# Performance work log

Measured on AMD Instinct MI355X. Metric: run time of the kernel, lower is better.

The kernel has to match this reference:

```python
import jax, jax.numpy as jnp
import numpy as np

L, M, DCUT, HL = 8, 8, 6, 2   # lattice rows, cols, bond dim, local Hilbert dim
N = L * M                     # nqubits
B = 32768                     # batch of spin configurations


def setup_inputs() -> dict:
    key = jax.random.key(0)
    ks = jax.random.split(key, 8)
    s = 0.1
    return {
        "parm_M_h": jax.random.normal(ks[0], (L, M, HL, DCUT, DCUT), jnp.float32) * s,
        "parm_M_v": jax.random.normal(ks[1], (L, M, HL, DCUT, DCUT), jnp.float32) * s,
        "parm_v":   jax.random.normal(ks[2], (L, M, HL, DCUT), jnp.float32) * s,
        "parm_T":   jax.random.normal(ks[3], (L, M, HL, DCUT, DCUT, DCUT), jnp.float32) * s,
        "parm_w":   jax.random.normal(ks[4], (L, M, DCUT), jnp.float32) * s,
        "parm_c":   jnp.zeros((L, M), jnp.float32),
        "parm_eta": jax.random.normal(ks[5], (L, M, DCUT), jnp.float32),
        "x":        jax.random.randint(ks[6], (B, N), 0, 2, jnp.int32),  # occupation bits 0/1
    }


def _snake_ij():
    # snake traversal: row i left->right if i even, right->left if i odd
    i = np.repeat(np.arange(L), M)
    jm = np.tile(np.arange(M), L)
    j = np.where(i % 2 == 0, jm, M - 1 - jm)
    return i, j


def _forward(parm_M_h, parm_M_v, parm_v, parm_T, parm_w, parm_c, parm_eta, x):
    target = x.T.astype(jnp.int32)               # (N, B) bits, qubit k visited at scan step k
    ii, jj = _snake_ij()
    # gather per-site params in snake scan order -> leading axis N
    Mh = parm_M_h[ii, jj]; Mv = parm_M_v[ii, jj]; V = parm_v[ii, jj]
    T = parm_T[ii, jj];    W = parm_w[ii, jj];    C = parm_c[ii, jj]
    Eta = parm_eta[ii, jj]
    jcol = jnp.asarray(jj, jnp.int32)            # column index per step (vertical state slot)
    row_start = jnp.asarray(np.arange(N) % M == 0)

    def step(carry, xs):
        h_h, v_state, amp, phi = carry
        Mh_k, Mv_k, V_k, T_k, W_k, C_k, eta_k, t_k, j_k, rs = xs
        # left boundary (ones) at the start of each row
        h_h = jnp.where(rs, 1.0, h_h)                                  # (dcut, B)
        h_v = jax.lax.dynamic_index_in_dim(v_state, j_k, 0, keepdims=False)  # (dcut, B)
        # update_h: residual small einsums ('abc,bd->acd' in torch)
        hh2 = h_h[None] + jnp.einsum('aoc,cb->aob', Mh_k, h_h)          # (hl, dcut, B)
        hv2 = h_v[None] + jnp.einsum('aoc,cb->aob', Mv_k, h_v)
        tt = jnp.einsum('aocd,cb,db->aob', T_k, h_h, h_v)               # tensor term
        h_full = hh2 + hv2 + tt + V_k[:, :, None]
        # normalize hidden per sample for numerical stability
        h_full = h_full / jnp.sqrt(jnp.sum(h_full * h_full, axis=(0, 1), keepdims=True) + 1e-12)
        # conditional probabilities P(s) ~ sum_o eta_o^2 h[s,o]^2
        q = jnp.einsum('o,aob->ab', eta_k * eta_k, h_full * h_full)     # (hl, B)
        prob = q / jnp.sum(q, axis=0, keepdims=True)
        sel = (t_k == 1)
        p_sel = jnp.where(sel, prob[1], prob[0])
        h_sel = jnp.where(sel[None, :], h_full[1], h_full[0])           # (dcut, B)
        amp = amp * jnp.sqrt(p_sel)
        phi = phi + jnp.einsum('o,ob->b', W_k, h_sel) + C_k             # regular phase accumulation
        v_state = jax.lax.dynamic_update_index_in_dim(v_state, h_sel, j_k, 0)
        return (h_sel, v_state, amp, phi), None

    h0 = jnp.ones((DCUT, B), jnp.float32)
    v0 = jnp.zeros((M, DCUT, B), jnp.float32)   # bottom boundary: zeros
    amp0 = jnp.ones((B,), jnp.float32)
    phi0 = jnp.zeros((B,), jnp.float32)
    (_, _, amp, phi), _ = jax.lax.scan(
        step, (h0, v0, amp0, phi0),
        (Mh, Mv, V, T, W, C, Eta, target, jcol, row_start))
    return amp, phi


def reference(parm_M_h, parm_M_v, parm_v, parm_T, parm_w, parm_c, parm_eta, x):
    amp, phi = _forward(parm_M_h, parm_M_v, parm_v, parm_T, parm_w, parm_c, parm_eta, x)
    # psi = amp * exp(i*phi)
    return amp * jnp.cos(phi) + 1j * (amp * jnp.sin(phi))
```

## Files before the change

### kernel.cpp

```cpp
#include <hip/hip_runtime.h>
#include <hip/hip_fp16.h>
#include <math.h>


#define NQ  64
#define BT  256
#define SPB 64
#define CHUNK_U 5184

typedef _Float16 h2v __attribute__((ext_vector_type(2)));
typedef __fp16  p2v __attribute__((ext_vector_type(2)));
union H2U { unsigned u; h2v h; __half2 hh; };

static __device__ __forceinline__ h2v pack2(float a, float b) {
    p2v p = __builtin_amdgcn_cvt_pkrtz(a, b);
    h2v r; __builtin_memcpy(&r, &p, sizeof(r));
    return r;
}
static __device__ __forceinline__ h2v u2h(unsigned u) {
    h2v r; __builtin_memcpy(&r, &u, sizeof(r));
    return r;
}
static __device__ __forceinline__ unsigned h2u(h2v h) {
    unsigned r; __builtin_memcpy(&r, &h, sizeof(r));
    return r;
}

#define DPPF(x, ctrl) __int_as_float(__builtin_amdgcn_update_dpp(            \
    __float_as_int(x), __float_as_int(x), (ctrl), 0xF, 0xF, false))
#define QP_XOR1 0xB1
#define QP_XOR2 0x4E
#define QP_BC0  0x00
#define QP_BC1  0x55

#if defined(__has_builtin)
#  if __has_builtin(__builtin_amdgcn_rcpf)
#    define FAST_RCP(x) __builtin_amdgcn_rcpf(x)
#  else
#    define FAST_RCP(x) (1.0f / (x))
#  endif
#  if __has_builtin(__builtin_amdgcn_rsqf)
#    define FAST_RSQ(x) __builtin_amdgcn_rsqf(x)
#  else
#    define FAST_RSQ(x) rsqrtf(x)
#  endif
#  if __has_builtin(__builtin_amdgcn_fdot2)
#    define HAS_FDOT2 1
#  endif
#else
#  define FAST_RCP(x) (1.0f / (x))
#  define FAST_RSQ(x) rsqrtf(x)
#endif

static __device__ __forceinline__ float fdot2u(unsigned a, h2v b, float c) {
#ifdef HAS_FDOT2
    H2U u; u.u = a;
    return __builtin_amdgcn_fdot2(u.h, b, c, false);
#else
    H2U u; u.u = a;
    return fmaf((float)u.h.x, (float)b.x, fmaf((float)u.h.y, (float)b.y, c));
#endif
}

__global__ void repack_k(
    const float* __restrict__ Mh, const float* __restrict__ Mv,
    const float* __restrict__ Vp, const float* __restrict__ Tp,
    const float* __restrict__ Wp, const float* __restrict__ Cp,
    const float* __restrict__ Ep, unsigned* __restrict__ ws)
{
    const int ch = blockIdx.x;
    const int t  = threadIdx.x;
    unsigned* Tm = ws + ch * CHUNK_U;
    float*    VE = reinterpret_cast<float*>(Tm + 4608);
    uint4*    Wl = reinterpret_cast<uint4*>(Tm + 4608 + 512);

    const float2* gT = reinterpret_cast<const float2*>(Tp + ch * 6912);
    for (int p = t; p < 3456; p += BT) {
        int site = p / 216, rr = p - site * 216;
        int row = rr / 18,  w  = rr - row * 18;
        float2 v = gT[p];
        H2U hu; hu.hh = __floats2half2_rn(v.x, v.y);
        Tm[(site * 12 + row) * 24 + w] = hu.u;
    }
    const float2* gH = reinterpret_cast<const float2*>(Mh + ch * 1152);
    const float2* gV = reinterpret_cast<const float2*>(Mv + ch * 1152);
    for (int p = t; p < 576; p += BT) {
        int site = p / 36, rr = p - site * 36;
        int row = rr / 3,  w  = rr - row * 3;
        int o_r = row - ((row >= 6) ? 6 : 0);
        float2 vh = gH[p], vv2 = gV[p];
        if ((o_r >> 1) == w) {
            if (o_r & 1) { vh.y += 1.f; vv2.y += 1.f; }
            else         { vh.x += 1.f; vv2.x += 1.f; }
        }
        H2U a; a.hh = __floats2half2_rn(vh.x, vh.y);
        H2U c; c.hh = __floats2half2_rn(vv2.x, vv2.y);
        Tm[(site * 12 + row) * 24 + 18 + w] = a.u;
        Tm[(site * 12 + row) * 24 + 21 + w] = c.u;
    }
    if (t < 192) {
        int site = t / 12, q = t - site * 12;
        int sb = q / 3,    c = q - sb * 3;
        VE[(site * 4 + sb) * 8 + c] = Vp[ch * 192 + t];
        float e = Ep[ch * 96 + site * 6 + (sb & 1) * 3 + c];
        VE[(site * 4 + sb) * 8 + 3 + c] = e * e;
    } else if (t < 208) {
        int site = t - 192;
        const float2* gw = reinterpret_cast<const float2*>(Wp) + ch * 48 + site * 3;
        float2 w01 = gw[0], w23 = gw[1], w45 = gw[2];
        H2U u0, u1, u2;
        u0.hh = __floats2half2_rn(w01.x, w01.y);
        u1.hh = __floats2half2_rn(w23.x, w23.y);
        u2.hh = __floats2half2_rn(w45.x, w45.y);
        Wl[site] = make_uint4(u0.u, u1.u, u2.u,
                              __float_as_uint(Cp[ch * 16 + site]));
    }
}

__global__ __launch_bounds__(BT, 1) void mps_rnn20(
    const unsigned* __restrict__ ws,
    const int* __restrict__ X,
    float* __restrict__ out, int Bn, int writeImag)
{
    __shared__ uint4    ldsb[CHUNK_U / 4];
    __shared__ unsigned vsm[8 * 64 * 4];

    unsigned*     Tl = reinterpret_cast<unsigned*>(ldsb);
    const float*  VE = reinterpret_cast<const float*>(Tl + 4608);
    const uint4*  Wl = reinterpret_cast<const uint4*>(Tl + 4608 + 512);

    const int t   = threadIdx.x;
    const int sub = t & 3;
    const int s   = t >> 2;
    int b = blockIdx.x * SPB + s;
    const bool valid = (b < Bn);
    if (!valid) b = Bn - 1;

    unsigned long long bits;
    {
        const int4* xr = reinterpret_cast<const int4*>(X + (size_t)b * NQ + sub * 16);
        unsigned long long part = 0ull;
        #pragma unroll
        for (int q = 0; q < 4; ++q) {
            int4 v = xr[q];
            part |= (unsigned long long)(v.x & 1) << (4 * q + 0);
            part |= (unsigned long long)(v.y & 1) << (4 * q + 1);
            part |= (unsigned long long)(v.z & 1) << (4 * q + 2);
            part |= (unsigned long long)(v.w & 1) << (4 * q + 3);
        }
        bits = part << (16 * sub);
        bits |= __shfl_xor(bits, 1, 64);
        bits |= __shfl_xor(bits, 2, 64);
    }

    for (int u = t; u < 8 * 64 * 4; u += BT) vsm[u] = 0u;

    const int mya = sub >> 1;

    float hh[6];
    h2v hhp0, hhp1, hhp2;
    float amp2 = 1.f, phi = 0.f;

    for (int ch = 0; ch < 4; ++ch) {
        __syncthreads();
        {
            const uint4* g4 = reinterpret_cast<const uint4*>(ws + ch * CHUNK_U);
            #pragma unroll
            for (int i = 0; i < 6; ++i) {
                int idx = t + i * BT;
                if (idx < CHUNK_U / 4) ldsb[idx] = g4[idx];
            }
        }
        __syncthreads();

        #pragma unroll
        for (int ih = 0; ih < 2; ++ih) {
            const unsigned cbr = (unsigned)(bits >> (ch * 16 + ih * 8)) & 0xFFu;

            #pragma unroll 2
            for (int qq = 0; qq < 8; ++qq) {
                const int j    = ih ? 7 - qq : qq;
                const int slot = ih * 8 + j;

                const unsigned* Tb = Tl + (slot * 12 + sub * 3) * 24;
                const float*   VEb = VE + (slot * 4 + sub) * 8;

                h2v hvh0, hvh1, hvh2;
                if (qq == 0) {
                    if (ch == 0 && ih == 0) {
                        H2U z; z.u = 0u;
                        hvh0 = z.h; hvh1 = z.h; hvh2 = z.h;
                    } else {
                        hvh0 = hhp0; hvh1 = hhp1; hvh2 = hhp2;
                    }
                    #pragma unroll
                    for (int o = 0; o < 6; ++o) hh[o] = 1.f;
                    H2U one; one.u = 0x3C003C00u;
                    hhp0 = one.h; hhp1 = one.h; hhp2 = one.h;
                } else {
                    uint4 hvu = *reinterpret_cast<const uint4*>(vsm + j * 256 + s * 4);
                    hvh0 = u2h(hvu.x); hvh1 = u2h(hvu.y); hvh2 = u2h(hvu.z);
                }

                float4 ve0 = *reinterpret_cast<const float4*>(VEb);
                float2 ve1 = *reinterpret_cast<const float2*>(VEb + 4);
                const float vv_[3] = { ve0.x, ve0.y, ve0.z };
                const float e2_[3] = { ve0.w, ve1.x, ve1.y };

                float acc[3];
                #pragma unroll
                for (int lr = 0; lr < 3; ++lr) {
                    const unsigned* Tr = Tb + lr * 24;
                    uint4 tA = *reinterpret_cast<const uint4*>(Tr);
                    uint4 tB = *reinterpret_cast<const uint4*>(Tr + 4);
                    uint4 tC = *reinterpret_cast<const uint4*>(Tr + 8);
                    uint4 tD = *reinterpret_cast<const uint4*>(Tr + 12);
                    uint4 tE = *reinterpret_cast<const uint4*>(Tr + 16);
                    uint4 tF = *reinterpret_cast<const uint4*>(Tr + 20);
                    const unsigned tw[18] = {tA.x,tA.y,tA.z,tA.w, tB.x,tB.y,tB.z,tB.w,
                                             tC.x,tC.y,tC.z,tC.w, tD.x,tD.y,tD.z,tD.w,
                                             tE.x,tE.y};
                    float sc[6];
                    #pragma unroll
                    for (int c = 0; c < 6; ++c)
                        sc[c] = fdot2u(tw[c*3+0], hvh0,
                                fdot2u(tw[c*3+1], hvh1,
                                fdot2u(tw[c*3+2], hvh2, 0.f)));

                    float ta = fmaf(sc[0], hh[0], fmaf(sc[2], hh[2], sc[4]*hh[4]));
                    float tb = fmaf(sc[1], hh[1], fmaf(sc[3], hh[3], sc[5]*hh[5]));
                    float md = fdot2u(tE.z, hhp0, fdot2u(tE.w, hhp1,
                               fdot2u(tF.x, hhp2, vv_[lr])));
                    float nd = fdot2u(tF.y, hvh0, fdot2u(tF.z, hvh1,
                               fdot2u(tF.w, hvh2, 0.f)));
                    acc[lr] = (ta + tb) + (md + nd);
                }

                float q0_ = acc[0]*acc[0], q1_ = acc[1]*acc[1], q2_ = acc[2]*acc[2];
                float ssl = (q0_ + q1_) + q2_;
                float pq  = fmaf(e2_[0], q0_, fmaf(e2_[1], q1_, e2_[2] * q2_));
                float s1  = ssl + DPPF(ssl, QP_XOR1);
                float ssq = s1 + DPPF(s1, QP_XOR2);
                float p1  = pq + DPPF(pq, QP_XOR1);
                float px  = DPPF(p1, QP_XOR2);
                const float inv = FAST_RSQ(ssq + 1e-12f);

                const int sel = (cbr >> qq) & 1;
                const float qsel = (mya == sel) ? p1 : px;
                amp2 *= qsel * FAST_RCP(p1 + px);

                float an0 = acc[0] * inv, an1 = acc[1] * inv, an2 = acc[2] * inv;
                float sw0 = DPPF(an0, QP_XOR2);
                float sw1 = DPPF(an1, QP_XOR2);
                float sw2 = DPPF(an2, QP_XOR2);
                an0 = sel ? sw0 : an0;
                an1 = sel ? sw1 : an1;
                an2 = sel ? sw2 : an2;
                hh[0] = DPPF(an0, QP_BC0); hh[3] = DPPF(an0, QP_BC1);
                hh[1] = DPPF(an1, QP_BC0); hh[4] = DPPF(an1, QP_BC1);
                hh[2] = DPPF(an2, QP_BC0); hh[5] = DPPF(an2, QP_BC1);
                hhp0 = pack2(hh[0], hh[1]);
                hhp1 = pack2(hh[2], hh[3]);
                hhp2 = pack2(hh[4], hh[5]);

                uint4 wv = Wl[slot];
                phi = fdot2u(wv.x, hhp0, fdot2u(wv.y, hhp1,
                      fdot2u(wv.z, hhp2, __uint_as_float(wv.w) + phi)));

                if (sub == 0 && qq != 7) {
                    *reinterpret_cast<uint4*>(vsm + j * 256 + s * 4) =
                        make_uint4(h2u(hhp0), h2u(hhp1), h2u(hhp2), 0u);
                }
            }
        }
    }

    if (sub == 0 && valid) {
        const float amp = sqrtf(amp2);
        if (writeImag) {
            out[2 * b + 0] = amp * cosf(phi);
            out[2 * b + 1] = amp * sinf(phi);
        } else {
            out[b] = amp * cosf(phi);
        }
    }
}

__global__ __launch_bounds__(BT, 1) void mps_rnn16fb(
    const float* __restrict__ Mh, const float* __restrict__ Mv,
    const float* __restrict__ Vp, const float* __restrict__ Tp,
    const float* __restrict__ Wp, const float* __restrict__ Cp,
    const float* __restrict__ Ep, const int* __restrict__ X,
    float* __restrict__ out, int Bn, int writeImag)
{
    __shared__ unsigned Tl[16 * 12 * 24];
    __shared__ float    VE [16 * 4 * 8];
    __shared__ uint4    Wl [16];
    __shared__ unsigned vsm[8 * 64 * 4];

    const int t   = threadIdx.x;
    const int sub = t & 3;
    const int s   = t >> 2;
    int b = blockIdx.x * SPB + s;
    const bool valid = (b < Bn);
    if (!valid) b = Bn - 1;

    unsigned long long bits;
    {
        const int4* xr = reinterpret_cast<const int4*>(X + (size_t)b * NQ + sub * 16);
        unsigned long long part = 0ull;
        #pragma unroll
        for (int q = 0; q < 4; ++q) {
            int4 v = xr[q];
            part |= (unsigned long long)(v.x & 1) << (4 * q + 0);
            part |= (unsigned long long)(v.y & 1) << (4 * q + 1);
            part |= (unsigned long long)(v.z & 1) << (4 * q + 2);
            part |= (unsigned long long)(v.w & 1) << (4 * q + 3);
        }
        bits = part << (16 * sub);
        bits |= __shfl_xor(bits, 1, 64);
        bits |= __shfl_xor(bits, 2, 64);
    }
    for (int u = t; u < 8 * 64 * 4; u += BT) vsm[u] = 0u;
    const int mya = sub >> 1;
    float hh[6];
    h2v hhp0, hhp1, hhp2;
    float amp2 = 1.f, phi = 0.f;

    for (int ch = 0; ch < 4; ++ch) {
        __syncthreads();
        {
            const float2* gT = reinterpret_cast<const float2*>(Tp + ch * 6912);
            for (int p = t; p < 3456; p += BT) {
                int site = p / 216, rr = p - site * 216;
                int row = rr / 18,  w  = rr - row * 18;
                float2 v = gT[p];
                H2U hu; hu.hh = __floats2half2_rn(v.x, v.y);
                Tl[(site * 12 + row) * 24 + w] = hu.u;
            }
            const float2* gH = reinterpret_cast<const float2*>(Mh + ch * 1152);
            const float2* gV = reinterpret_cast<const float2*>(Mv + ch * 1152);
            for (int p = t; p < 576; p += BT) {
                int site = p / 36, rr = p - site * 36;
                int row = rr / 3,  w  = rr - row * 3;
                int o_r = row - ((row >= 6) ? 6 : 0);
                float2 vh = gH[p], vv2 = gV[p];
                if ((o_r >> 1) == w) {
                    if (o_r & 1) { vh.y += 1.f; vv2.y += 1.f; }
                    else         { vh.x += 1.f; vv2.x += 1.f; }
                }
                H2U a; a.hh = __floats2half2_rn(vh.x, vh.y);
                H2U c; c.hh = __floats2half2_rn(vv2.x, vv2.y);
                Tl[(site * 12 + row) * 24 + 18 + w] = a.u;
                Tl[(site * 12 + row) * 24 + 21 + w] = c.u;
            }
            if (t < 192) {
                int site = t / 12, q = t - site * 12;
                int sb = q / 3,    c = q - sb * 3;
                VE[(site * 4 + sb) * 8 + c] = Vp[ch * 192 + t];
                float e = Ep[ch * 96 + site * 6 + (sb & 1) * 3 + c];
                VE[(site * 4 + sb) * 8 + 3 + c] = e * e;
            } else if (t < 208) {
                int site = t - 192;
                const float2* gw = reinterpret_cast<const float2*>(Wp) + ch * 48 + site * 3;
                float2 w01 = gw[0], w23 = gw[1], w45 = gw[2];
                H2U u0, u1, u2;
                u0.hh = __floats2half2_rn(w01.x, w01.y);
                u1.hh = __floats2half2_rn(w23.x, w23.y);
                u2.hh = __floats2half2_rn(w45.x, w45.y);
                Wl[site] = make_uint4(u0.u, u1.u, u2.u,
                                      __float_as_uint(Cp[ch * 16 + site]));
            }
        }
        __syncthreads();

        #pragma unroll
        for (int ih = 0; ih < 2; ++ih) {
            const unsigned cbr = (unsigned)(bits >> (ch * 16 + ih * 8)) & 0xFFu;
            #pragma unroll 2
            for (int qq = 0; qq < 8; ++qq) {
                const int j    = ih ? 7 - qq : qq;
                const int slot = ih * 8 + j;
                const unsigned* Tb = Tl + (slot * 12 + sub * 3) * 24;
                const float*   VEb = VE + (slot * 4 + sub) * 8;
                if (qq == 0) {
                    #pragma unroll
                    for (int o = 0; o < 6; ++o) hh[o] = 1.f;
                    H2U one; one.u = 0x3C003C00u;
                    hhp0 = one.h; hhp1 = one.h; hhp2 = one.h;
                }
                uint4 hvu = *reinterpret_cast<const uint4*>(vsm + j * 256 + s * 4);
                const h2v hvh0 = u2h(hvu.x);
                const h2v hvh1 = u2h(hvu.y);
                const h2v hvh2 = u2h(hvu.z);
                float4 ve0 = *reinterpret_cast<const float4*>(VEb);
                float2 ve1 = *reinterpret_cast<const float2*>(VEb + 4);
                const float vv_[3] = { ve0.x, ve0.y, ve0.z };
                const float e2_[3] = { ve0.w, ve1.x, ve1.y };
                float acc[3];
                #pragma unroll
                for (int lr = 0; lr < 3; ++lr) {
                    const unsigned* Tr = Tb + lr * 24;
                    uint4 tA = *reinterpret_cast<const uint4*>(Tr);
                    uint4 tB = *reinterpret_cast<const uint4*>(Tr + 4);
                    uint4 tC = *reinterpret_cast<const uint4*>(Tr + 8);
                    uint4 tD = *reinterpret_cast<const uint4*>(Tr + 12);
                    uint4 tE = *reinterpret_cast<const uint4*>(Tr + 16);
                    uint4 tF = *reinterpret_cast<const uint4*>(Tr + 20);
                    const unsigned tw[18] = {tA.x,tA.y,tA.z,tA.w, tB.x,tB.y,tB.z,tB.w,
                                             tC.x,tC.y,tC.z,tC.w, tD.x,tD.y,tD.z,tD.w,
                                             tE.x,tE.y};
                    float sc[6];
                    #pragma unroll
                    for (int c = 0; c < 6; ++c)
                        sc[c] = fdot2u(tw[c*3+0], hvh0,
                                fdot2u(tw[c*3+1], hvh1,
                                fdot2u(tw[c*3+2], hvh2, 0.f)));
                    float ta = fmaf(sc[0], hh[0], fmaf(sc[2], hh[2], sc[4]*hh[4]));
                    float tb = fmaf(sc[1], hh[1], fmaf(sc[3], hh[3], sc[5]*hh[5]));
                    float md = fdot2u(tE.z, hhp0, fdot2u(tE.w, hhp1,
                               fdot2u(tF.x, hhp2, vv_[lr])));
                    float nd = fdot2u(tF.y, hvh0, fdot2u(tF.z, hvh1,
                               fdot2u(tF.w, hvh2, 0.f)));
                    acc[lr] = (ta + tb) + (md + nd);
                }
                float q0_ = acc[0]*acc[0], q1_ = acc[1]*acc[1], q2_ = acc[2]*acc[2];
                float ssl = (q0_ + q1_) + q2_;
                float pq  = fmaf(e2_[0], q0_, fmaf(e2_[1], q1_, e2_[2] * q2_));
                float s1  = ssl + DPPF(ssl, QP_XOR1);
                float ssq = s1 + DPPF(s1, QP_XOR2);
                float p1  = pq + DPPF(pq, QP_XOR1);
                float px  = DPPF(p1, QP_XOR2);
                const float inv = FAST_RSQ(ssq + 1e-12f);
                const int sel = (cbr >> qq) & 1;
                const float qsel = (mya == sel) ? p1 : px;
                amp2 *= qsel * FAST_RCP(p1 + px);
                float an0 = acc[0] * inv, an1 = acc[1] * inv, an2 = acc[2] * inv;
                float sw0 = DPPF(an0, QP_XOR2);
                float sw1 = DPPF(an1, QP_XOR2);
                float sw2 = DPPF(an2, QP_XOR2);
                an0 = sel ? sw0 : an0;
                an1 = sel ? sw1 : an1;
                an2 = sel ? sw2 : an2;
                hh[0] = DPPF(an0, QP_BC0); hh[3] = DPPF(an0, QP_BC1);
                hh[1] = DPPF(an1, QP_BC0); hh[4] = DPPF(an1, QP_BC1);
                hh[2] = DPPF(an2, QP_BC0); hh[5] = DPPF(an2, QP_BC1);
                hhp0 = pack2(hh[0], hh[1]);
                hhp1 = pack2(hh[2], hh[3]);
                hhp2 = pack2(hh[4], hh[5]);
                uint4 wv = Wl[slot];
                phi = fdot2u(wv.x, hhp0, fdot2u(wv.y, hhp1,
                      fdot2u(wv.z, hhp2, __uint_as_float(wv.w) + phi)));
                if (sub == 0) {
                    *reinterpret_cast<uint4*>(vsm + j * 256 + s * 4) =
                        make_uint4(h2u(hhp0), h2u(hhp1), h2u(hhp2), 0u);
                }
            }
        }
    }

    if (sub == 0 && valid) {
        const float amp = sqrtf(amp2);
        if (writeImag) {
            out[2 * b + 0] = amp * cosf(phi);
            out[2 * b + 1] = amp * sinf(phi);
        } else {
            out[b] = amp * cosf(phi);
        }
    }
}

extern "C" void kernel_launch(void* const* d_in, const int* in_sizes, int n_in,
                              void* d_out, int out_size, void* d_ws, size_t ws_size,
                              hipStream_t stream) {
    const float* Mh = (const float*)d_in[0];
    const float* Mv = (const float*)d_in[1];
    const float* Vp = (const float*)d_in[2];
    const float* Tp = (const float*)d_in[3];
    const float* Wp = (const float*)d_in[4];
    const float* Cp = (const float*)d_in[5];
    const float* Ep = (const float*)d_in[6];
    const int*   X  = (const int*)d_in[7];
    float* out = (float*)d_out;

    const int Bn = in_sizes[7] / NQ;
    const int writeImag = (out_size >= 2 * Bn) ? 1 : 0;
    const int grid = (Bn + SPB - 1) / SPB;

    const size_t need = (size_t)4 * CHUNK_U * sizeof(unsigned);
    if (ws_size >= need) {
        repack_k<<<4, BT, 0, stream>>>(Mh, Mv, Vp, Tp, Wp, Cp, Ep,
                                       (unsigned*)d_ws);
        mps_rnn20<<<grid, BT, 0, stream>>>((const unsigned*)d_ws, X, out,
                                           Bn, writeImag);
    } else {
        mps_rnn16fb<<<grid, BT, 0, stream>>>(Mh, Mv, Vp, Tp, Wp, Cp, Ep, X,
                                             out, Bn, writeImag);
    }
}
```

Before: 63.33 us.

## Process two batch samples per quad to reuse T weights loaded from LDS

The main kernel now handles 128 samples per block instead of 64, with each 4-lane quad carrying two independent sample chains (A and B) through the snake scan. Each T-row LDS load is shared by both chains, which halves the number of LDS weight reads per sample and also halves the number of chunk staging passes and barriers per sample. The two independent dependency chains give the scheduler more instruction-level parallelism. In exchange the grid is halved to 256 blocks, so fewer waves run concurrently, and register pressure roughly doubles.

```diff
diff --git a/kernel.cpp b/kernel.cpp
--- a/kernel.cpp
+++ b/kernel.cpp
@@ -5,7 +5,6 @@
 
 #define NQ  64
 #define BT  256
-#define SPB 64
 #define CHUNK_U 5184
 
 typedef _Float16 h2v __attribute__((ext_vector_type(2)));
@@ -117,13 +116,32 @@
     }
 }
 
-__global__ __launch_bounds__(BT, 1) void mps_rnn20(
+static __device__ __forceinline__ unsigned long long pack_bits(
+    const int* X, int b, int sub)
+{
+    const int4* xr = reinterpret_cast<const int4*>(X + (size_t)b * NQ + sub * 16);
+    unsigned long long part = 0ull;
+    #pragma unroll
+    for (int q = 0; q < 4; ++q) {
+        int4 v = xr[q];
+        part |= (unsigned long long)(v.x & 1) << (4 * q + 0);
+        part |= (unsigned long long)(v.y & 1) << (4 * q + 1);
+        part |= (unsigned long long)(v.z & 1) << (4 * q + 2);
+        part |= (unsigned long long)(v.w & 1) << (4 * q + 3);
+    }
+    unsigned long long bits = part << (16 * sub);
+    bits |= __shfl_xor(bits, 1, 64);
+    bits |= __shfl_xor(bits, 2, 64);
+    return bits;
+}
+
+__global__ __launch_bounds__(BT, 1) void mps_rnn21(
     const unsigned* __restrict__ ws,
     const int* __restrict__ X,
     float* __restrict__ out, int Bn, int writeImag)
 {
     __shared__ uint4    ldsb[CHUNK_U / 4];
-    __shared__ unsigned vsm[8 * 64 * 4];
+    __shared__ unsigned vsm[8 * 128 * 4];
 
     unsigned*     Tl = reinterpret_cast<unsigned*>(ldsb);
     const float*  VE = reinterpret_cast<const float*>(Tl + 4608);
@@ -132,34 +150,22 @@
     const int t   = threadIdx.x;
     const int sub = t & 3;
     const int s   = t >> 2;
-    int b = blockIdx.x * SPB + s;
-    const bool valid = (b < Bn);
-    if (!valid) b = Bn - 1;
-
-    unsigned long long bits;
-    {
-        const int4* xr = reinterpret_cast<const int4*>(X + (size_t)b * NQ + sub * 16);
-        unsigned long long part = 0ull;
-        #pragma unroll
-        for (int q = 0; q < 4; ++q) {
-            int4 v = xr[q];
-            part |= (unsigned long long)(v.x & 1) << (4 * q + 0);
-            part |= (unsigned long long)(v.y & 1) << (4 * q + 1);
-            part |= (unsigned long long)(v.z & 1) << (4 * q + 2);
-            part |= (unsigned long long)(v.w & 1) << (4 * q + 3);
-        }
-        bits = part << (16 * sub);
-        bits |= __shfl_xor(bits, 1, 64);
-        bits |= __shfl_xor(bits, 2, 64);
-    }
-
-    for (int u = t; u < 8 * 64 * 4; u += BT) vsm[u] = 0u;
+    int bA = blockIdx.x * 128 + s;
+    int bB = bA + 64;
+    const bool vA = (bA < Bn), vB = (bB < Bn);
+    if (!vA) bA = Bn - 1;
+    if (!vB) bB = Bn - 1;
+
+    const unsigned long long bitsA = pack_bits(X, bA, sub);
+    const unsigned long long bitsB = pack_bits(X, bB, sub);
+
+    for (int u = t; u < 8 * 128 * 4; u += BT) vsm[u] = 0u;
 
     const int mya = sub >> 1;
 
-    float hh[6];
-    h2v hhp0, hhp1, hhp2;
-    float amp2 = 1.f, phi = 0.f;
+    float hhA[6], hhB[6];
+    h2v hap0, hap1, hap2, hbp0, hbp1, hbp2;
+    float amp2A = 1.f, phiA = 0.f, amp2B = 1.f, phiB = 0.f;
 
     for (int ch = 0; ch < 4; ++ch) {
         __syncthreads();
@@ -175,7 +181,8 @@
 
         #pragma unroll
         for (int ih = 0; ih < 2; ++ih) {
-            const unsigned cbr = (unsigned)(bits >> (ch * 16 + ih * 8)) & 0xFFu;
+            const unsigned cbrA = (unsigned)(bitsA >> (ch * 16 + ih * 8)) & 0xFFu;
+            const unsigned cbrB = (unsigned)(bitsB >> (ch * 16 + ih * 8)) & 0xFFu;
 
             #pragma unroll 2
             for (int qq = 0; qq < 8; ++qq) {
@@ -185,21 +192,26 @@
                 const unsigned* Tb = Tl + (slot * 12 + sub * 3) * 24;
                 const float*   VEb = VE + (slot * 4 + sub) * 8;
 
-                h2v hvh0, hvh1, hvh2;
+                h2v va0, va1, va2, vb0, vb1, vb2;
                 if (qq == 0) {
                     if (ch == 0 && ih == 0) {
                         H2U z; z.u = 0u;
-                        hvh0 = z.h; hvh1 = z.h; hvh2 = z.h;
+                        va0 = z.h; va1 = z.h; va2 = z.h;
+                        vb0 = z.h; vb1 = z.h; vb2 = z.h;
                     } else {
-                        hvh0 = hhp0; hvh1 = hhp1; hvh2 = hhp2;
+                        va0 = hap0; va1 = hap1; va2 = hap2;
+                        vb0 = hbp0; vb1 = hbp1; vb2 = hbp2;
                     }
                     #pragma unroll
-                    for (int o = 0; o < 6; ++o) hh[o] = 1.f;
+                    for (int o = 0; o < 6; ++o) { hhA[o] = 1.f; hhB[o] = 1.f; }
                     H2U one; one.u = 0x3C003C00u;
-                    hhp0 = one.h; hhp1 = one.h; hhp2 = one.h;
+                    hap0 = one.h; hap1 = one.h; hap2 = one.h;
+                    hbp0 = one.h; hbp1 = one.h; hbp2 = one.h;
                 } else {
-                    uint4 hvu = *reinterpret_cast<const uint4*>(vsm + j * 256 + s * 4);
-                    hvh0 = u2h(hvu.x); hvh1 = u2h(hvu.y); hvh2 = u2h(hvu.z);
+                    uint4 ha = *reinterpret_cast<const uint4*>(vsm + j * 512 + s * 4);
+                    uint4 hb = *reinterpret_cast<const uint4*>(vsm + j * 512 + (s + 64) * 4);
+                    va0 = u2h(ha.x); va1 = u2h(ha.y); va2 = u2h(ha.z);
+                    vb0 = u2h(hb.x); vb1 = u2h(hb.y); vb2 = u2h(hb.z);
                 }
 
                 float4 ve0 = *reinterpret_cast<const float4*>(VEb);
@@ -207,81 +219,128 @@
                 const float vv_[3] = { ve0.x, ve0.y, ve0.z };
                 const float e2_[3] = { ve0.w, ve1.x, ve1.y };
 
-                float acc[3];
+                float accA[3], accB[3];
                 #pragma unroll
                 for (int lr = 0; lr < 3; ++lr) {
                     const unsigned* Tr = Tb + lr * 24;
-                    uint4 tA = *reinterpret_cast<const uint4*>(Tr);
-                    uint4 tB = *reinterpret_cast<const uint4*>(Tr + 4);
-                    uint4 tC = *reinterpret_cast<const uint4*>(Tr + 8);
-                    uint4 tD = *reinterpret_cast<const uint4*>(Tr + 12);
-                    uint4 tE = *reinterpret_cast<const uint4*>(Tr + 16);
-                    uint4 tF = *reinterpret_cast<const uint4*>(Tr + 20);
-                    const unsigned tw[18] = {tA.x,tA.y,tA.z,tA.w, tB.x,tB.y,tB.z,tB.w,
-                                             tC.x,tC.y,tC.z,tC.w, tD.x,tD.y,tD.z,tD.w,
-                                             tE.x,tE.y};
-                    float sc[6];
+                    uint4 tA4 = *reinterpret_cast<const uint4*>(Tr);
+                    uint4 tB4 = *reinterpret_cast<const uint4*>(Tr + 4);
+                    uint4 tC4 = *reinterpret_cast<const uint4*>(Tr + 8);
+                    uint4 tD4 = *reinterpret_cast<const uint4*>(Tr + 12);
+                    uint4 tE4 = *reinterpret_cast<const uint4*>(Tr + 16);
+                    uint4 tF4 = *reinterpret_cast<const uint4*>(Tr + 20);
+                    const unsigned tw[18] = {tA4.x,tA4.y,tA4.z,tA4.w,
+                                             tB4.x,tB4.y,tB4.z,tB4.w,
+                                             tC4.x,tC4.y,tC4.z,tC4.w,
+                                             tD4.x,tD4.y,tD4.z,tD4.w,
+                                             tE4.x,tE4.y};
+                    float scA[6];
                     #pragma unroll
                     for (int c = 0; c < 6; ++c)
-                        sc[c] = fdot2u(tw[c*3+0], hvh0,
-                                fdot2u(tw[c*3+1], hvh1,
-                                fdot2u(tw[c*3+2], hvh2, 0.f)));
-
-                    float ta = fmaf(sc[0], hh[0], fmaf(sc[2], hh[2], sc[4]*hh[4]));
-                    float tb = fmaf(sc[1], hh[1], fmaf(sc[3], hh[3], sc[5]*hh[5]));
-                    float md = fdot2u(tE.z, hhp0, fdot2u(tE.w, hhp1,
-                               fdot2u(tF.x, hhp2, vv_[lr])));
-                    float nd = fdot2u(tF.y, hvh0, fdot2u(tF.z, hvh1,
-                               fdot2u(tF.w, hvh2, 0.f)));
-                    acc[lr] = (ta + tb) + (md + nd);
-                }
-
-                float q0_ = acc[0]*acc[0], q1_ = acc[1]*acc[1], q2_ = acc[2]*acc[2];
-                float ssl = (q0_ + q1_) + q2_;
-                float pq  = fmaf(e2_[0], q0_, fmaf(e2_[1], q1_, e2_[2] * q2_));
-                float s1  = ssl + DPPF(ssl, QP_XOR1);
-                float ssq = s1 + DPPF(s1, QP_XOR2);
-                float p1  = pq + DPPF(pq, QP_XOR1);
-                float px  = DPPF(p1, QP_XOR2);
-                const float inv = FAST_RSQ(ssq + 1e-12f);
-
-                const int sel = (cbr >> qq) & 1;
-                const float qsel = (mya == sel) ? p1 : px;
-                amp2 *= qsel * FAST_RCP(p1 + px);
-
-                float an0 = acc[0] * inv, an1 = acc[1] * inv, an2 = acc[2] * inv;
-                float sw0 = DPPF(an0, QP_XOR2);
-                float sw1 = DPPF(an1, QP_XOR2);
-                float sw2 = DPPF(an2, QP_XOR2);
-                an0 = sel ? sw0 : an0;
-                an1 = sel ? sw1 : an1;
-                an2 = sel ? sw2 : an2;
-                hh[0] = DPPF(an0, QP_BC0); hh[3] = DPPF(an0, QP_BC1);
-                hh[1] = DPPF(an1, QP_BC0); hh[4] = DPPF(an1, QP_BC1);
-                hh[2] = DPPF(an2, QP_BC0); hh[5] = DPPF(an2, QP_BC1);
-                hhp0 = pack2(hh[0], hh[1]);
-                hhp1 = pack2(hh[2], hh[3]);
-                hhp2 = pack2(hh[4], hh[5]);
-
-                uint4 wv = Wl[slot];
-                phi = fdot2u(wv.x, hhp0, fdot2u(wv.y, hhp1,
-                      fdot2u(wv.z, hhp2, __uint_as_float(wv.w) + phi)));
+                        scA[c] = fdot2u(tw[c*3+0], va0,
+                                 fdot2u(tw[c*3+1], va1,
+                                 fdot2u(tw[c*3+2], va2, 0.f)));
+                    float taA = fmaf(scA[0], hhA[0], fmaf(scA[2], hhA[2], scA[4]*hhA[4]));
+                    float tbA = fmaf(scA[1], hhA[1], fmaf(scA[3], hhA[3], scA[5]*hhA[5]));
+                    float mdA = fdot2u(tE4.z, hap0, fdot2u(tE4.w, hap1,
+                                fdot2u(tF4.x, hap2, vv_[lr])));
+                    float ndA = fdot2u(tF4.y, va0, fdot2u(tF4.z, va1,
+                                fdot2u(tF4.w, va2, 0.f)));
+                    accA[lr] = (taA + tbA) + (mdA + ndA);
+                    float scB[6];
+                    #pragma unroll
+                    for (int c = 0; c < 6; ++c)
+                        scB[c] = fdot2u(tw[c*3+0], vb0,
+                                 fdot2u(tw[c*3+1], vb1,
+                                 fdot2u(tw[c*3+2], vb2, 0.f)));
+                    float taB = fmaf(scB[0], hhB[0], fmaf(scB[2], hhB[2], scB[4]*hhB[4]));
+                    float tbB = fmaf(scB[1], hhB[1], fmaf(scB[3], hhB[3], scB[5]*hhB[5]));
+                    float mdB = fdot2u(tE4.z, hbp0, fdot2u(tE4.w, hbp1,
+                                fdot2u(tF4.x, hbp2, vv_[lr])));
+                    float ndB = fdot2u(tF4.y, vb0, fdot2u(tF4.z, vb1,
+                                fdot2u(tF4.w, vb2, 0.f)));
+                    accB[lr] = (taB + tbB) + (mdB + ndB);
+                }
+
+                const uint4 wv = Wl[slot];
+                const int selA = (cbrA >> qq) & 1;
+                const int selB = (cbrB >> qq) & 1;
+
+                {
+                    float q0 = accA[0]*accA[0], q1 = accA[1]*accA[1], q2 = accA[2]*accA[2];
+                    float ssl = (q0 + q1) + q2;
+                    float pq  = fmaf(e2_[0], q0, fmaf(e2_[1], q1, e2_[2] * q2));
+                    float s1  = ssl + DPPF(ssl, QP_XOR1);
+                    float ssq = s1 + DPPF(s1, QP_XOR2);
+                    float p1  = pq + DPPF(pq, QP_XOR1);
+                    float px  = DPPF(p1, QP_XOR2);
+                    const float inv = FAST_RSQ(ssq + 1e-12f);
+                    const float qsel = (mya == selA) ? p1 : px;
+                    amp2A *= qsel * FAST_RCP(p1 + px);
+                    float a0 = accA[0]*inv, a1 = accA[1]*inv, a2 = accA[2]*inv;
+                    float w0 = DPPF(a0, QP_XOR2), w1 = DPPF(a1, QP_XOR2), w2 = DPPF(a2, QP_XOR2);
+                    a0 = selA ? w0 : a0; a1 = selA ? w1 : a1; a2 = selA ? w2 : a2;
+                    hhA[0] = DPPF(a0, QP_BC0); hhA[3] = DPPF(a0, QP_BC1);
+                    hhA[1] = DPPF(a1, QP_BC0); hhA[4] = DPPF(a1, QP_BC1);
+                    hhA[2] = DPPF(a2, QP_BC0); hhA[5] = DPPF(a2, QP_BC1);
+                    hap0 = pack2(hhA[0], hhA[1]);
+                    hap1 = pack2(hhA[2], hhA[3]);
+                    hap2 = pack2(hhA[4], hhA[5]);
+                    phiA = fdot2u(wv.x, hap0, fdot2u(wv.y, hap1,
+                           fdot2u(wv.z, hap2, __uint_as_float(wv.w) + phiA)));
+                }
+                {
+                    float q0 = accB[0]*accB[0], q1 = accB[1]*accB[1], q2 = accB[2]*accB[2];
+                    float ssl = (q0 + q1) + q2;
+                    float pq  = fmaf(e2_[0], q0, fmaf(e2_[1], q1, e2_[2] * q2));
+                    float s1  = ssl + DPPF(ssl, QP_XOR1);
+                    float ssq = s1 + DPPF(s1, QP_XOR2);
+                    float p1  = pq + DPPF(pq, QP_XOR1);
+                    float px  = DPPF(p1, QP_XOR2);
+                    const float inv = FAST_RSQ(ssq + 1e-12f);
+                    const float qsel = (mya == selB) ? p1 : px;
+                    amp2B *= qsel * FAST_RCP(p1 + px);
+                    float a0 = accB[0]*inv, a1 = accB[1]*inv, a2 = accB[2]*inv;
+                    float w0 = DPPF(a0, QP_XOR2), w1 = DPPF(a1, QP_XOR2), w2 = DPPF(a2, QP_XOR2);
+                    a0 = selB ? w0 : a0; a1 = selB ? w1 : a1; a2 = selB ? w2 : a2;
+                    hhB[0] = DPPF(a0, QP_BC0); hhB[3] = DPPF(a0, QP_BC1);
+                    hhB[1] = DPPF(a1, QP_BC0); hhB[4] = DPPF(a1, QP_BC1);
+                    hhB[2] = DPPF(a2, QP_BC0); hhB[5] = DPPF(a2, QP_BC1);
+                    hbp0 = pack2(hhB[0], hhB[1]);
+                    hbp1 = pack2(hhB[2], hhB[3]);
+                    hbp2 = pack2(hhB[4], hhB[5]);
+                    phiB = fdot2u(wv.x, hbp0, fdot2u(wv.y, hbp1,
+                           fdot2u(wv.z, hbp2, __uint_as_float(wv.w) + phiB)));
+                }
 
                 if (sub == 0 && qq != 7) {
-                    *reinterpret_cast<uint4*>(vsm + j * 256 + s * 4) =
-                        make_uint4(h2u(hhp0), h2u(hhp1), h2u(hhp2), 0u);
-                }
-            }
-        }
-    }
-
-    if (sub == 0 && valid) {
-        const float amp = sqrtf(amp2);
-        if (writeImag) {
-            out[2 * b + 0] = amp * cosf(phi);
-            out[2 * b + 1] = amp * sinf(phi);
-        } else {
-            out[b] = amp * cosf(phi);
+                    *reinterpret_cast<uint4*>(vsm + j * 512 + s * 4) =
+                        make_uint4(h2u(hap0), h2u(hap1), h2u(hap2), 0u);
+                    *reinterpret_cast<uint4*>(vsm + j * 512 + (s + 64) * 4) =
+                        make_uint4(h2u(hbp0), h2u(hbp1), h2u(hbp2), 0u);
+                }
+            }
+        }
+    }
+
+    if (sub == 0) {
+        if (vA) {
+            const float amp = sqrtf(amp2A);
+            if (writeImag) {
+                out[2 * bA + 0] = amp * cosf(phiA);
+                out[2 * bA + 1] = amp * sinf(phiA);
+            } else {
+                out[bA] = amp * cosf(phiA);
+            }
+        }
+        if (vB) {
+            const float amp = sqrtf(amp2B);
+            if (writeImag) {
+                out[2 * bB + 0] = amp * cosf(phiB);
+                out[2 * bB + 1] = amp * sinf(phiB);
+            } else {
+                out[bB] = amp * cosf(phiB);
+            }
         }
     }
 }
@@ -301,26 +360,11 @@
     const int t   = threadIdx.x;
     const int sub = t & 3;
     const int s   = t >> 2;
-    int b = blockIdx.x * SPB + s;
+    int b = blockIdx.x * 64 + s;
     const bool valid = (b < Bn);
     if (!valid) b = Bn - 1;
 
-    unsigned long long bits;
-    {
-        const int4* xr = reinterpret_cast<const int4*>(X + (size_t)b * NQ + sub * 16);
-        unsigned long long part = 0ull;
-        #pragma unroll
-        for (int q = 0; q < 4; ++q) {
-            int4 v = xr[q];
-            part |= (unsigned long long)(v.x & 1) << (4 * q + 0);
-            part |= (unsigned long long)(v.y & 1) << (4 * q + 1);
-            part |= (unsigned long long)(v.z & 1) << (4 * q + 2);
-            part |= (unsigned long long)(v.w & 1) << (4 * q + 3);
-        }
-        bits = part << (16 * sub);
-        bits |= __shfl_xor(bits, 1, 64);
-        bits |= __shfl_xor(bits, 2, 64);
-    }
+    unsigned long long bits = pack_bits(X, b, sub);
     for (int u = t; u < 8 * 64 * 4; u += BT) vsm[u] = 0u;
     const int mya = sub >> 1;
     float hh[6];
@@ -485,15 +529,16 @@
 
     const int Bn = in_sizes[7] / NQ;
     const int writeImag = (out_size >= 2 * Bn) ? 1 : 0;
-    const int grid = (Bn + SPB - 1) / SPB;
 
     const size_t need = (size_t)4 * CHUNK_U * sizeof(unsigned);
     if (ws_size >= need) {
         repack_k<<<4, BT, 0, stream>>>(Mh, Mv, Vp, Tp, Wp, Cp, Ep,
                                        (unsigned*)d_ws);
-        mps_rnn20<<<grid, BT, 0, stream>>>((const unsigned*)d_ws, X, out,
+        const int grid = (Bn + 127) / 128;
+        mps_rnn21<<<grid, BT, 0, stream>>>((const unsigned*)d_ws, X, out,
                                            Bn, writeImag);
     } else {
+        const int grid = (Bn + 63) / 64;
         mps_rnn16fb<<<grid, BT, 0, stream>>>(Mh, Mv, Vp, Tp, Wp, Cp, Ep, X,
                                              out, Bn, writeImag);
     }
```

New measurement: 69.32 us. 1.09x slower.

## Split per-site weight rows between LDS and direct global/cache loads

Applied to the files above, without the earlier changes.

Repacks each site's weight rows into two planes. The first half of the T words stays staged in LDS together with V/eta and W/C. The remaining T words plus the Mh/Mv identity-shifted words are read straight from global memory (through cache) inside the inner loop. This halves the LDS footprint and the per-chunk cooperative copy, cutting LDS traffic and staging time. The cost is per-iteration global/L1 loads with higher latency in the hot loop.

```diff
diff --git a/kernel.cpp b/kernel.cpp
--- a/kernel.cpp
+++ b/kernel.cpp
@@ -70,9 +70,10 @@
 {
     const int ch = blockIdx.x;
     const int t  = threadIdx.x;
-    unsigned* Tm = ws + ch * CHUNK_U;
-    float*    VE = reinterpret_cast<float*>(Tm + 4608);
-    uint4*    Wl = reinterpret_cast<uint4*>(Tm + 4608 + 512);
+    unsigned* P0 = ws + ch * CHUNK_U;
+    float*    VE = reinterpret_cast<float*>(P0 + 2304);
+    uint4*    Wl = reinterpret_cast<uint4*>(P0 + 2816);
+    unsigned* P1 = P0 + 2880;
 
     const float2* gT = reinterpret_cast<const float2*>(Tp + ch * 6912);
     for (int p = t; p < 3456; p += BT) {
@@ -80,7 +81,9 @@
         int row = rr / 18,  w  = rr - row * 18;
         float2 v = gT[p];
         H2U hu; hu.hh = __floats2half2_rn(v.x, v.y);
-        Tm[(site * 12 + row) * 24 + w] = hu.u;
+        int ri = site * 12 + row;
+        if (w < 12) P0[ri * 12 + w]        = hu.u;
+        else        P1[ri * 12 + (w - 12)] = hu.u;
     }
     const float2* gH = reinterpret_cast<const float2*>(Mh + ch * 1152);
     const float2* gV = reinterpret_cast<const float2*>(Mv + ch * 1152);
@@ -95,8 +98,9 @@
         }
         H2U a; a.hh = __floats2half2_rn(vh.x, vh.y);
         H2U c; c.hh = __floats2half2_rn(vv2.x, vv2.y);
-        Tm[(site * 12 + row) * 24 + 18 + w] = a.u;
-        Tm[(site * 12 + row) * 24 + 21 + w] = c.u;
+        int ri = site * 12 + row;
+        P1[ri * 12 + 6 + w] = a.u;
+        P1[ri * 12 + 9 + w] = c.u;
     }
     if (t < 192) {
         int site = t / 12, q = t - site * 12;
@@ -117,17 +121,17 @@
     }
 }
 
-__global__ __launch_bounds__(BT, 1) void mps_rnn20(
+__global__ __launch_bounds__(BT, 1) void mps_rnn22(
     const unsigned* __restrict__ ws,
     const int* __restrict__ X,
     float* __restrict__ out, int Bn, int writeImag)
 {
-    __shared__ uint4    ldsb[CHUNK_U / 4];
+    __shared__ uint4    ldsb[720];
     __shared__ unsigned vsm[8 * 64 * 4];
 
     unsigned*     Tl = reinterpret_cast<unsigned*>(ldsb);
-    const float*  VE = reinterpret_cast<const float*>(Tl + 4608);
-    const uint4*  Wl = reinterpret_cast<const uint4*>(Tl + 4608 + 512);
+    const float*  VE = reinterpret_cast<const float*>(Tl + 2304);
+    const uint4*  Wl = reinterpret_cast<const uint4*>(Tl + 2816);
 
     const int t   = threadIdx.x;
     const int sub = t & 3;
@@ -166,12 +170,14 @@
         {
             const uint4* g4 = reinterpret_cast<const uint4*>(ws + ch * CHUNK_U);
             #pragma unroll
-            for (int i = 0; i < 6; ++i) {
+            for (int i = 0; i < 3; ++i) {
                 int idx = t + i * BT;
-                if (idx < CHUNK_U / 4) ldsb[idx] = g4[idx];
+                if (idx < 720) ldsb[idx] = g4[idx];
             }
         }
         __syncthreads();
+
+        const uint4* G1c = reinterpret_cast<const uint4*>(ws + ch * CHUNK_U + 2880);
 
         #pragma unroll
         for (int ih = 0; ih < 2; ++ih) {
@@ -182,7 +188,8 @@
                 const int j    = ih ? 7 - qq : qq;
                 const int slot = ih * 8 + j;
 
-                const unsigned* Tb = Tl + (slot * 12 + sub * 3) * 24;
+                const unsigned* Tb = Tl + (slot * 12 + sub * 3) * 12;
+                const uint4*    G1 = G1c + (slot * 12 + sub * 3) * 3;
                 const float*   VEb = VE + (slot * 4 + sub) * 8;
 
                 h2v hvh0, hvh1, hvh2;
@@ -210,13 +217,12 @@
                 float acc[3];
                 #pragma unroll
                 for (int lr = 0; lr < 3; ++lr) {
-                    const unsigned* Tr = Tb + lr * 24;
-                    uint4 tA = *reinterpret_cast<const uint4*>(Tr);
-                    uint4 tB = *reinterpret_cast<const uint4*>(Tr + 4);
-                    uint4 tC = *reinterpret_cast<const uint4*>(Tr + 8);
-                    uint4 tD = *reinterpret_cast<const uint4*>(Tr + 12);
-                    uint4 tE = *reinterpret_cast<const uint4*>(Tr + 16);
-                    uint4 tF = *reinterpret_cast<const uint4*>(Tr + 20);
+                    uint4 tA = *reinterpret_cast<const uint4*>(Tb + lr * 12);
+                    uint4 tB = *reinterpret_cast<const uint4*>(Tb + lr * 12 + 4);
+                    uint4 tC = *reinterpret_cast<const uint4*>(Tb + lr * 12 + 8);
+                    uint4 tD = G1[lr * 3 + 0];
+                    uint4 tE = G1[lr * 3 + 1];
+                    uint4 tF = G1[lr * 3 + 2];
                     const unsigned tw[18] = {tA.x,tA.y,tA.z,tA.w, tB.x,tB.y,tB.z,tB.w,
                                              tC.x,tC.y,tC.z,tC.w, tD.x,tD.y,tD.z,tD.w,
                                              tE.x,tE.y};
@@ -491,7 +497,7 @@
     if (ws_size >= need) {
         repack_k<<<4, BT, 0, stream>>>(Mh, Mv, Vp, Tp, Wp, Cp, Ep,
                                        (unsigned*)d_ws);
-        mps_rnn20<<<grid, BT, 0, stream>>>((const unsigned*)d_ws, X, out,
+        mps_rnn22<<<grid, BT, 0, stream>>>((const unsigned*)d_ws, X, out,
                                            Bn, writeImag);
     } else {
         mps_rnn16fb<<<grid, BT, 0, stream>>>(Mh, Mv, Vp, Tp, Wp, Cp, Ep, X,
```

Result: slower. 75.37 us (+19.0%).
